# Optimization experiments

Hardware: AMD Instinct MI355X
Metric: run time of the kernel (lower is better)

Reference implementation:

```python
import jax, jax.numpy as jnp
import numpy as np

DN = ('NHWC', 'HWIO', 'NHWC')

def _conv1x1(x, k):
    # 1x1 conv, stride 1, SAME padding (channels_last)
    return jax.lax.conv_general_dilated(x, k, window_strides=(1, 1), padding='SAME', dimension_numbers=DN)

def setup_inputs() -> dict:
    key = jax.random.key(0)
    k1, k2, k3, k4, k5 = jax.random.split(key, 5)
    B, H, W, C = 4, 64, 64, 256
    c8 = C // 8
    x = jax.random.normal(k1, (B, H, W, C), dtype=jnp.float32)
    # Glorot-like scaling for stability
    kernel_f = jax.random.normal(k2, (1, 1, C, c8), dtype=jnp.float32) * (1.0 / np.sqrt(C))
    kernel_g = jax.random.normal(k3, (1, 1, C, c8), dtype=jnp.float32) * (1.0 / np.sqrt(C))
    kernel_h = jax.random.normal(k4, (1, 1, C, C), dtype=jnp.float32) * (1.0 / np.sqrt(C))
    gamma = jax.random.normal(k5, (), dtype=jnp.float32) * 0.1
    return {'x': x, 'kernel_f': kernel_f, 'kernel_g': kernel_g, 'kernel_h': kernel_h, 'gamma': gamma}

def reference(x, kernel_f, kernel_g, kernel_h, gamma):
    B, H, W, C = x.shape
    N = H * W
    f = _conv1x1(x, kernel_f).reshape(B, N, -1)   # [B, N, C/8] queries
    g = _conv1x1(x, kernel_g).reshape(B, N, -1)   # [B, N, C/8] keys
    h = _conv1x1(x, kernel_h).reshape(B, N, -1)   # [B, N, C]   values
    e = jnp.einsum('bnc,bmc->bnm', f, g)          # [B, N, N] scores
    attn = jax.nn.softmax(e, axis=-1)
    o = jnp.einsum('bnm,bmc->bnc', attn, h).reshape(B, H, W, C)
    return x + gamma * o
```

## Files before the change

### kernel.cpp

```cpp
#include <hip/hip_runtime.h>

typedef __attribute__((ext_vector_type(8))) short bf16x8;
typedef __attribute__((ext_vector_type(4))) float f32x4;
typedef __attribute__((ext_vector_type(16))) float f32x16;

__device__ __forceinline__ unsigned short f2bf(float f) {
    union { float f; unsigned u; } v; v.f = f;
    return (unsigned short)((v.u + 0x7FFFu + ((v.u >> 16) & 1u)) >> 16);
}
__device__ __forceinline__ unsigned f2bf2_fast(float a, float b) {
    union { float f; unsigned u; } va, vb; va.f = a; vb.f = b;
    return ((va.u + 0x8000u) >> 16) | ((vb.u + 0x8000u) & 0xFFFF0000u);
}

__device__ __forceinline__ void async16(unsigned short* lds, const unsigned short* gsrc) {
    __builtin_amdgcn_global_load_lds(
        (const __attribute__((address_space(1))) void*)gsrc,
        (__attribute__((address_space(3))) void*)lds, 16, 0, 0);
}

__global__ __launch_bounds__(256) void k_wt(const float* __restrict__ kf,
                                            const float* __restrict__ kg,
                                            const float* __restrict__ kh,
                                            unsigned short* __restrict__ wt) {
    int n = blockIdx.x, t = threadIdx.x;
    const float* src; int stride, col;
    if (n < 32)      { src = kf; stride = 32;  col = n; }
    else if (n < 64) { src = kg; stride = 32;  col = n - 32; }
    else             { src = kh; stride = 256; col = n - 64; }
    wt[n * 256 + (((t >> 3) ^ (n & 7)) << 3) + (t & 7)] = f2bf(src[t * stride + col]);
}

__global__ __launch_bounds__(512) void k_proj(const float* __restrict__ x,
                                              const unsigned short* __restrict__ wt,
                                              unsigned short* __restrict__ f,
                                              unsigned short* __restrict__ g,
                                              unsigned short* __restrict__ hT) {
    __shared__ unsigned short xs[16384];
    __shared__ unsigned short ws[2][16384];
    int t = threadIdx.x, rb = blockIdx.x;
    int w = t >> 6, lane = t & 63, q = lane >> 4, n15 = lane & 15;
    int b = rb >> 6, nbase = (rb & 63) * 64;

#pragma unroll
    for (int i = 0; i < 8; ++i) {
        int lin = i * 512 + t, row = lin >> 6, c4 = lin & 63;
        float4 v = *(const float4*)&x[(rb * 64 + row) * 256 + c4 * 4];
        ushort4 o; o.x = f2bf(v.x); o.y = f2bf(v.y); o.z = f2bf(v.z); o.w = f2bf(v.w);
        *(ushort4*)&xs[row * 256 + (((c4 >> 1) ^ (row & 7)) << 3) + ((c4 & 1) << 2)] = o;
    }
#pragma unroll
    for (int j = 0; j < 4; ++j)
        async16(&ws[0][(j * 512 + w * 64) * 8], wt + (j * 512 + t) * 8);

    for (int ct = 0; ct < 5; ++ct) {
        int cur = ct & 1, nxt = cur ^ 1;
        __syncthreads();
        if (ct < 4) {
            const unsigned short* wsrc = wt + (ct + 1) * 16384;
#pragma unroll
            for (int j = 0; j < 4; ++j)
                async16(&ws[nxt][(j * 512 + w * 64) * 8], wsrc + (j * 512 + t) * 8);
        }
        const unsigned short* wcur = ws[cur];
        f32x4 acc[2];
        acc[0] = (f32x4){0.f, 0.f, 0.f, 0.f};
        acc[1] = (f32x4){0.f, 0.f, 0.f, 0.f};

        if (ct == 0) {
            int rg = w & 3, cg = w >> 2;
#pragma unroll
            for (int kk = 0; kk < 8; ++kk) {
                bf16x8 a = *(const bf16x8*)&xs[(rg * 16 + n15) * 256
                                + ((((kk << 2) + q) ^ (n15 & 7)) << 3)];
#pragma unroll
                for (int nt = 0; nt < 2; ++nt) {
                    bf16x8 bw = *(const bf16x8*)&wcur[(cg * 32 + nt * 16 + n15) * 256
                                    + ((((kk << 2) + q) ^ (n15 & 7)) << 3)];
                    acc[nt] = __builtin_amdgcn_mfma_f32_16x16x32_bf16(a, bw, acc[nt], 0, 0, 0);
                }
            }
#pragma unroll
            for (int nt = 0; nt < 2; ++nt)
#pragma unroll
                for (int r = 0; r < 4; ++r) {
                    int grow = rb * 64 + rg * 16 + q * 4 + r;
                    int col = cg * 32 + nt * 16 + n15;
                    unsigned short v = f2bf(acc[nt][r]);
                    if (col < 32) f[grow * 32 + col] = v;
                    else          g[grow * 32 + (col - 32)] = v;
                }
        } else {
            int cg = w & 3, rg = w >> 2;
#pragma unroll
            for (int kk = 0; kk < 8; ++kk) {
                bf16x8 a = *(const bf16x8*)&wcur[(cg * 16 + n15) * 256
                                + ((((kk << 2) + q) ^ (n15 & 7)) << 3)];
#pragma unroll
                for (int nt = 0; nt < 2; ++nt) {
                    bf16x8 bx = *(const bf16x8*)&xs[(rg * 32 + nt * 16 + n15) * 256
                                    + ((((kk << 2) + q) ^ (n15 & 7)) << 3)];
                    acc[nt] = __builtin_amdgcn_mfma_f32_16x16x32_bf16(a, bx, acc[nt], 0, 0, 0);
                }
            }
#pragma unroll
            for (int nt = 0; nt < 2; ++nt)
#pragma unroll
                for (int r = 0; r < 4; ++r) {
                    int ch = (ct - 1) * 64 + cg * 16 + q * 4 + r;
                    int nloc = nbase + rg * 32 + nt * 16 + n15;
                    hT[b * 1048576 + ch * 4096 + nloc] = f2bf(acc[nt][r]);
                }
        }
    }
}

__global__ __launch_bounds__(512, 4) void k_attn(const float* __restrict__ x,
                                                 const unsigned short* __restrict__ f,
                                                 const unsigned short* __restrict__ g,
                                                 const unsigned short* __restrict__ hT,
                                                 const float* __restrict__ gamma_p,
                                                 float* __restrict__ out) {
    __shared__ unsigned short hs[2][8192];
    __shared__ unsigned short pls[2][4096];
    __shared__ float lrec[64];
    int t = threadIdx.x, bx = blockIdx.x;
    int b = (bx >> 1) & 3;
    int ch2 = (bx >> 3) & 1;
    int qt = ((bx & 1) << 5) | (bx >> 4);
    int qbase = qt * 64;
    int chbase = ch2 * 128;
    int w = t >> 6, l = t & 63;
    int hi = l >> 5, l31 = l & 31;
    int q = l >> 4, n15 = l & 15;
    int rw = w & 1, cw = (w >> 1) & 3;
    const bool is_s = (w < 4);

    bf16x8 aFB;
    if (is_s)
        aFB = *(const bf16x8*)&f[(b * 4096 + qbase + w * 16 + n15) * 32 + q * 8];

    const unsigned short* hsrc = hT + b * 1048576 + (chbase + (t >> 3)) * 4096
                               + (((t & 7) ^ ((t >> 3) & 7)) << 3);

    const unsigned short* gbase = g + (b * 4096 + n15) * 32 + q * 8;
    bf16x8 aG[4], aGn[4];

    f32x16 o;
#pragma unroll
    for (int i = 0; i < 16; ++i) o[i] = 0.f;
    float l_acc = 0.f;
    const f32x4 zero4 = (f32x4){0.f, 0.f, 0.f, 0.f};

    auto s_tile = [&](int buf) {
        f32x4 sa[4];
#pragma unroll
        for (int nt = 0; nt < 4; ++nt)
            sa[nt] = __builtin_amdgcn_mfma_f32_16x16x32_bf16(aG[nt], aFB, zero4, 0, 0, 0);
#pragma unroll
        for (int nt = 0; nt < 4; ++nt)
#pragma unroll
            for (int r = 0; r < 4; ++r) {
                sa[nt][r] = __expf(sa[nt][r]);
                l_acc += sa[nt][r];
            }
#pragma unroll
        for (int nt = 0; nt < 4; ++nt) {
            unsigned p0 = f2bf2_fast(sa[nt][0], sa[nt][1]);
            unsigned p1 = f2bf2_fast(sa[nt][2], sa[nt][3]);
            int kq = 4 * nt + q;
            unsigned* dst = (unsigned*)&pls[buf][(w * 16 + n15) * 64]
                          + ((kq >> 1) ^ (n15 & 7)) * 4 + (kq & 1) * 2;
            dst[0] = p0; dst[1] = p1;
        }
    };

    async16(&hs[0][w * 512], hsrc);
    async16(&hs[0][4096 + w * 512], hsrc + 64 * 4096);
    if (is_s) {
#pragma unroll
        for (int nt = 0; nt < 4; ++nt)
            aG[nt] = *(const bf16x8*)&gbase[(nt * 16) * 32];
#pragma unroll
        for (int nt = 0; nt < 4; ++nt)
            aGn[nt] = *(const bf16x8*)&gbase[(64 + nt * 16) * 32];
        s_tile(0);
#pragma unroll
        for (int nt = 0; nt < 4; ++nt) aG[nt] = aGn[nt];
    }
    __syncthreads();

    for (int kt = 0; kt < 64; ++kt) {
        int cur = kt & 1, nxt = cur ^ 1;

        if (kt + 1 < 64) {
            const unsigned short* hp = hsrc + (kt + 1) * 64;
            async16(&hs[nxt][w * 512], hp);
            async16(&hs[nxt][4096 + w * 512], hp + 64 * 4096);
        }

        if (is_s && kt + 1 < 64) {
            int ktn = (kt + 2 < 64) ? kt + 2 : 63;
#pragma unroll
            for (int nt = 0; nt < 4; ++nt)
                aGn[nt] = *(const bf16x8*)&gbase[(ktn * 64 + nt * 16) * 32];
            s_tile(nxt);
#pragma unroll
            for (int nt = 0; nt < 4; ++nt) aG[nt] = aGn[nt];
        }

        const unsigned short* hcur = &hs[cur][0];
        const unsigned short* pcur = &pls[cur][0];
#pragma unroll
        for (int ks = 0; ks < 4; ++ks) {
            int seg = (((2 * ks + hi) ^ (l31 & 7)) << 3);
            bf16x8 aP = *(const bf16x8*)&pcur[(rw * 32 + l31) * 64 + seg];
            bf16x8 bH = *(const bf16x8*)&hcur[(cw * 32 + l31) * 64 + seg];
            o = __builtin_amdgcn_mfma_f32_32x32x16_bf16(aP, bH, o, 0, 0, 0);
        }

        __syncthreads();
    }

    if (is_s) {
        float ps = l_acc;
        ps += __shfl_xor(ps, 16);
        ps += __shfl_xor(ps, 32);
        if (q == 0) lrec[w * 16 + n15] = 1.0f / ps;
    }
    __syncthreads();
    float gam = *gamma_p;
#pragma unroll
    for (int qq = 0; qq < 4; ++qq) {
        f32x4 ri = *(const f32x4*)&lrec[rw * 32 + 8 * qq + 4 * hi];
#pragma unroll
        for (int j = 0; j < 4; ++j) {
            int row = qbase + rw * 32 + 8 * qq + 4 * hi + j;
            int ch = chbase + cw * 32 + l31;
            int idx = (b * 4096 + row) * 256 + ch;
            out[idx] = x[idx] + gam * (o[4 * qq + j] * ri[j]);
        }
    }
}

extern "C" void kernel_launch(void* const* d_in, const int* in_sizes, int n_in,
                              void* d_out, int out_size, void* d_ws, size_t ws_size,
                              hipStream_t stream) {
    const float* x  = (const float*)d_in[0];
    const float* kf = (const float*)d_in[1];
    const float* kg = (const float*)d_in[2];
    const float* kh = (const float*)d_in[3];
    const float* gm = (const float*)d_in[4];
    float* out = (float*)d_out;

    char* ws = (char*)d_ws;
    unsigned short* wt = (unsigned short*)(ws);
    unsigned short* fb = (unsigned short*)(ws + 163840);
    unsigned short* gb = (unsigned short*)(ws + 1212416);
    unsigned short* hT = (unsigned short*)(ws + 2260992);

    hipLaunchKernelGGL(k_wt,   dim3(320), dim3(256), 0, stream, kf, kg, kh, wt);
    hipLaunchKernelGGL(k_proj, dim3(256), dim3(512), 0, stream, x, wt, fb, gb, hT);
    hipLaunchKernelGGL(k_attn, dim3(512), dim3(512), 0, stream, x, fb, gb, hT, gm, out);
}
```

Baseline: 157.1 us.

## Specialize warps: score warps compute softmax tiles, PV warps do all MFMA

Waves 0-3 now only compute the score/exp tiles. Waves 4-7 take over the whole P·V accumulation, each owning a 32-channel strip over all 64 query rows with two accumulators. Before, every wave did a quarter of the PV MFMAs on top of the score work done by half of them. The aim is to stop the score waves from serializing softmax and PV work, so the two stages overlap across wave groups. In exchange the PV waves double their accumulator registers and MFMA load, and half the block sits idle in the epilogue.

```diff
diff --git a/kernel.cpp b/kernel.cpp
--- a/kernel.cpp
+++ b/kernel.cpp
@@ -133,7 +133,7 @@
     int w = t >> 6, l = t & 63;
     int hi = l >> 5, l31 = l & 31;
     int q = l >> 4, n15 = l & 15;
-    int rw = w & 1, cw = (w >> 1) & 3;
+    int cb = w & 3;
     const bool is_s = (w < 4);
 
     bf16x8 aFB;
@@ -146,9 +146,9 @@
     const unsigned short* gbase = g + (b * 4096 + n15) * 32 + q * 8;
     bf16x8 aG[4], aGn[4];
 
-    f32x16 o;
-#pragma unroll
-    for (int i = 0; i < 16; ++i) o[i] = 0.f;
+    f32x16 o0, o1;
+#pragma unroll
+    for (int i = 0; i < 16; ++i) { o0[i] = 0.f; o1[i] = 0.f; }
     float l_acc = 0.f;
     const f32x4 zero4 = (f32x4){0.f, 0.f, 0.f, 0.f};
 
@@ -199,24 +199,28 @@
             async16(&hs[nxt][4096 + w * 512], hp + 64 * 4096);
         }
 
-        if (is_s && kt + 1 < 64) {
-            int ktn = (kt + 2 < 64) ? kt + 2 : 63;
-#pragma unroll
-            for (int nt = 0; nt < 4; ++nt)
-                aGn[nt] = *(const bf16x8*)&gbase[(ktn * 64 + nt * 16) * 32];
-            s_tile(nxt);
-#pragma unroll
-            for (int nt = 0; nt < 4; ++nt) aG[nt] = aGn[nt];
-        }
-
-        const unsigned short* hcur = &hs[cur][0];
-        const unsigned short* pcur = &pls[cur][0];
-#pragma unroll
-        for (int ks = 0; ks < 4; ++ks) {
-            int seg = (((2 * ks + hi) ^ (l31 & 7)) << 3);
-            bf16x8 aP = *(const bf16x8*)&pcur[(rw * 32 + l31) * 64 + seg];
-            bf16x8 bH = *(const bf16x8*)&hcur[(cw * 32 + l31) * 64 + seg];
-            o = __builtin_amdgcn_mfma_f32_32x32x16_bf16(aP, bH, o, 0, 0, 0);
+        if (is_s) {
+            if (kt + 1 < 64) {
+                int ktn = (kt + 2 < 64) ? kt + 2 : 63;
+#pragma unroll
+                for (int nt = 0; nt < 4; ++nt)
+                    aGn[nt] = *(const bf16x8*)&gbase[(ktn * 64 + nt * 16) * 32];
+                s_tile(nxt);
+#pragma unroll
+                for (int nt = 0; nt < 4; ++nt) aG[nt] = aGn[nt];
+            }
+        } else {
+            const unsigned short* hcur = &hs[cur][0];
+            const unsigned short* pcur = &pls[cur][0];
+#pragma unroll
+            for (int ks = 0; ks < 4; ++ks) {
+                int seg = (((2 * ks + hi) ^ (l31 & 7)) << 3);
+                bf16x8 bH  = *(const bf16x8*)&hcur[(cb * 32 + l31) * 64 + seg];
+                bf16x8 aP0 = *(const bf16x8*)&pcur[l31 * 64 + seg];
+                bf16x8 aP1 = *(const bf16x8*)&pcur[(32 + l31) * 64 + seg];
+                o0 = __builtin_amdgcn_mfma_f32_32x32x16_bf16(aP0, bH, o0, 0, 0, 0);
+                o1 = __builtin_amdgcn_mfma_f32_32x32x16_bf16(aP1, bH, o1, 0, 0, 0);
+            }
         }
 
         __syncthreads();
@@ -229,16 +233,21 @@
         if (q == 0) lrec[w * 16 + n15] = 1.0f / ps;
     }
     __syncthreads();
-    float gam = *gamma_p;
-#pragma unroll
-    for (int qq = 0; qq < 4; ++qq) {
-        f32x4 ri = *(const f32x4*)&lrec[rw * 32 + 8 * qq + 4 * hi];
-#pragma unroll
-        for (int j = 0; j < 4; ++j) {
-            int row = qbase + rw * 32 + 8 * qq + 4 * hi + j;
-            int ch = chbase + cw * 32 + l31;
-            int idx = (b * 4096 + row) * 256 + ch;
-            out[idx] = x[idx] + gam * (o[4 * qq + j] * ri[j]);
+    if (!is_s) {
+        float gam = *gamma_p;
+        int ch = chbase + cb * 32 + l31;
+#pragma unroll
+        for (int qq = 0; qq < 4; ++qq) {
+            int r0 = 8 * qq + 4 * hi;
+            f32x4 ri0 = *(const f32x4*)&lrec[r0];
+            f32x4 ri1 = *(const f32x4*)&lrec[32 + r0];
+#pragma unroll
+            for (int j = 0; j < 4; ++j) {
+                int idx0 = (b * 4096 + qbase + r0 + j) * 256 + ch;
+                int idx1 = idx0 + 32 * 256;
+                out[idx0] = x[idx0] + gam * (o0[4 * qq + j] * ri0[j]);
+                out[idx1] = x[idx1] + gam * (o1[4 * qq + j] * ri1[j]);
+            }
         }
     }
 }
```

Measured after the change: 151.3 us. 1.04x faster.
